# Performance work log

Measured on AMD Instinct MI355X. Metric: run time of the kernel, lower is better.

The kernel has to match this reference:

```python
import jax, jax.numpy as jnp
import numpy as np

B, NK, TK, H = 16, 2048, 4096, 256


def setup_inputs() -> dict:
    key = jax.random.key(0)
    ks = jax.random.split(key, 9)
    s = 0.02  # init scale for weights
    return {
        "s_t_hat": jax.random.normal(ks[0], (B, 2 * H), dtype=jnp.float32),
        "encoder_outputs_node": jax.random.normal(ks[1], (B, NK, H), dtype=jnp.float32),
        "node_to_token": jax.random.uniform(ks[2], (B, NK, TK), dtype=jnp.float32),
        "enc_padding_mask_node": jnp.ones((B, NK), dtype=jnp.float32),
        "graph": jax.random.uniform(ks[3], (B, NK, NK), dtype=jnp.float32),
        "flow": jax.random.uniform(ks[4], (B, NK), dtype=jnp.float32),
        "W_c_w": jax.random.normal(ks[5], (1, H), dtype=jnp.float32) * s,
        "enc_proj_w": jax.random.normal(ks[6], (H, H), dtype=jnp.float32) * s,
        "dec_proj_w": jax.random.normal(ks[7], (2 * H, H), dtype=jnp.float32) * s,
        "dec_proj_b": jnp.zeros((H,), dtype=jnp.float32),
        "v_node_w": jax.random.normal(ks[8], (H, 1), dtype=jnp.float32) * s,
    }


def reference(s_t_hat, encoder_outputs_node, node_to_token, enc_padding_mask_node,
              graph, flow, W_c_w, enc_proj_w, dec_proj_w, dec_proj_b, v_node_w):
    # additive attention scoring over graph nodes
    enc_feat = jnp.einsum('bkh,hd->bkd', encoder_outputs_node, enc_proj_w)   # (b,nk,h)
    dec_fea = s_t_hat @ dec_proj_w + dec_proj_b                              # (b,h)
    _flow_feature = flow[..., None] @ W_c_w  # computed in original but unused (dead code)
    e = jnp.tanh(enc_feat + dec_fea[:, None, :])                             # (b,nk,h)
    scores = jnp.squeeze(e @ v_node_w, -1)                                   # (b,nk)
    # masked softmax with renormalization
    attn_ = jax.nn.softmax(scores, axis=1) * enc_padding_mask_node
    attn = attn_ / jnp.sum(attn_, axis=1, keepdims=True)                     # (b,nk)
    # project node attention to token space, renormalize
    tok_ = jnp.einsum('bk,bkt->bt', attn, node_to_token)                     # (b,tk)
    tok = tok_ / jnp.sum(tok_, axis=1, keepdims=True)
    # context vector
    c_t = jnp.einsum('bk,bkh->bh', attn, encoder_outputs_node)               # (b,h)
    # multi-hop graph diffusion
    one_hop = jnp.einsum('bk,bkm->bm', attn, graph)                          # (b,nk)
    two_hop = jnp.einsum('bk,bkm->bm', one_hop, graph)                       # (b,nk)
    flow_out = attn * 0.33333 + one_hop * 0.33333 + two_hop * 0.33333        # (b,nk)
    return (c_t, attn, tok, flow_out)
```

## Files before the change

### kernel.cpp

```cpp
#include <hip/hip_runtime.h>
#include <cstddef>

#define BB 16
#define NK 2048
#define TK 4096
#define HH 256
#define H2 512

__global__ void k_dec_fea(const float* __restrict__ s_t_hat,
                          const float* __restrict__ Wd,
                          const float* __restrict__ bd,
                          float* __restrict__ dec_fea) {
    int b = blockIdx.x, d = threadIdx.x;
    __shared__ float s[H2];
    s[d]       = s_t_hat[b * H2 + d];
    s[d + HH]  = s_t_hat[b * H2 + HH + d];
    __syncthreads();
    float acc = bd[d];
    #pragma unroll 8
    for (int j = 0; j < H2; ++j) acc = fmaf(s[j], Wd[j * HH + d], acc);
    dec_fea[b * HH + d] = acc;
}

__global__ void k_scores(const float* __restrict__ enc,
                         const float* __restrict__ Wenc,
                         const float* __restrict__ dec_fea,
                         const float* __restrict__ v,
                         float* __restrict__ scores) {
    int b   = blockIdx.y;
    int k0  = blockIdx.x * 16;
    int tid = threadIdx.x;
    int lane = tid & 63;
    int wv   = tid >> 6;

    __shared__ float4 encSV[16 * 64];
    const float4* baseV = (const float4*)(enc + ((size_t)b * NK + k0) * HH);
    #pragma unroll
    for (int r = 0; r < 4; ++r) encSV[r * 256 + tid] = baseV[r * 256 + tid];
    __syncthreads();

    const float4* Wv = (const float4*)Wenc;
    float4 acc[4];
    #pragma unroll
    for (int i = 0; i < 4; ++i) acc[i] = make_float4(0.f, 0.f, 0.f, 0.f);

    for (int h4 = 0; h4 < 64; ++h4) {
        float4 w0 = Wv[(h4 * 4 + 0) * 64 + lane];
        float4 w1 = Wv[(h4 * 4 + 1) * 64 + lane];
        float4 w2 = Wv[(h4 * 4 + 2) * 64 + lane];
        float4 w3 = Wv[(h4 * 4 + 3) * 64 + lane];
        #pragma unroll
        for (int i = 0; i < 4; ++i) {
            float4 e = encSV[(wv * 4 + i) * 64 + h4];
            acc[i].x = fmaf(e.x, w0.x, acc[i].x); acc[i].y = fmaf(e.x, w0.y, acc[i].y);
            acc[i].z = fmaf(e.x, w0.z, acc[i].z); acc[i].w = fmaf(e.x, w0.w, acc[i].w);
            acc[i].x = fmaf(e.y, w1.x, acc[i].x); acc[i].y = fmaf(e.y, w1.y, acc[i].y);
            acc[i].z = fmaf(e.y, w1.z, acc[i].z); acc[i].w = fmaf(e.y, w1.w, acc[i].w);
            acc[i].x = fmaf(e.z, w2.x, acc[i].x); acc[i].y = fmaf(e.z, w2.y, acc[i].y);
            acc[i].z = fmaf(e.z, w2.z, acc[i].z); acc[i].w = fmaf(e.z, w2.w, acc[i].w);
            acc[i].x = fmaf(e.w, w3.x, acc[i].x); acc[i].y = fmaf(e.w, w3.y, acc[i].y);
            acc[i].z = fmaf(e.w, w3.z, acc[i].z); acc[i].w = fmaf(e.w, w3.w, acc[i].w);
        }
    }

    float4 df = ((const float4*)(dec_fea + b * HH))[lane];
    float4 vv = ((const float4*)v)[lane];
    #pragma unroll
    for (int i = 0; i < 4; ++i) {
        float p = tanhf(acc[i].x + df.x) * vv.x
                + tanhf(acc[i].y + df.y) * vv.y
                + tanhf(acc[i].z + df.z) * vv.z
                + tanhf(acc[i].w + df.w) * vv.w;
        #pragma unroll
        for (int off = 32; off > 0; off >>= 1) p += __shfl_down(p, off, 64);
        if (lane == 0) scores[b * NK + k0 + wv * 4 + i] = p;
    }
}

__global__ void k_softmax(const float* __restrict__ scores,
                          const float* __restrict__ mask,
                          float* __restrict__ attn) {
    int b = blockIdx.x, tid = threadIdx.x;
    int lane = tid & 63, wv = tid >> 6;
    __shared__ float redmax[4], redsum[4];
    float vals[8];
    float m = -1e30f;
    #pragma unroll
    for (int r = 0; r < 8; ++r) {
        vals[r] = scores[b * NK + r * 256 + tid];
        m = fmaxf(m, vals[r]);
    }
    #pragma unroll
    for (int off = 1; off < 64; off <<= 1) m = fmaxf(m, __shfl_xor(m, off, 64));
    if (lane == 0) redmax[wv] = m;
    __syncthreads();
    m = fmaxf(fmaxf(redmax[0], redmax[1]), fmaxf(redmax[2], redmax[3]));
    float s = 0.f;
    #pragma unroll
    for (int r = 0; r < 8; ++r) {
        float e = __expf(vals[r] - m) * mask[b * NK + r * 256 + tid];
        vals[r] = e;
        s += e;
    }
    #pragma unroll
    for (int off = 1; off < 64; off <<= 1) s += __shfl_xor(s, off, 64);
    if (lane == 0) redsum[wv] = s;
    __syncthreads();
    s = redsum[0] + redsum[1] + redsum[2] + redsum[3];
    float inv = 1.f / s;
    #pragma unroll
    for (int r = 0; r < 8; ++r) attn[b * NK + r * 256 + tid] = vals[r] * inv;
}

__global__ void k_ct(const float* __restrict__ attn,
                     const float* __restrict__ enc,
                     float* __restrict__ out) {
    int b = blockIdx.y;
    int k0 = blockIdx.x * 64;
    int h = threadIdx.x;
    const float* e  = enc + ((size_t)b * NK + k0) * HH;
    const float* wb = attn + b * NK + k0;
    float acc = 0.f;
    #pragma unroll 8
    for (int k = 0; k < 64; ++k) acc = fmaf(wb[k], e[(size_t)k * HH + h], acc);
    atomicAdd(&out[b * HH + h], acc);
}

template <int NCOLS, int KCH>
__global__ void k_vecmat(const float* __restrict__ w,
                         const float* __restrict__ M,
                         float* __restrict__ out) {
    int b  = blockIdx.z;
    int k0 = blockIdx.y * (NK / KCH);
    int t  = blockIdx.x * 1024 + threadIdx.x * 4;
    const float4* Mv = (const float4*)(M + (size_t)b * NK * NCOLS);
    const float* wb  = w + b * NK;
    float4 acc = make_float4(0.f, 0.f, 0.f, 0.f);
    int kend = k0 + NK / KCH;
    #pragma unroll 4
    for (int k = k0; k < kend; ++k) {
        float a = wb[k];
        float4 vv = Mv[(size_t)k * (NCOLS / 4) + (t >> 2)];
        acc.x = fmaf(a, vv.x, acc.x);
        acc.y = fmaf(a, vv.y, acc.y);
        acc.z = fmaf(a, vv.z, acc.z);
        acc.w = fmaf(a, vv.w, acc.w);
    }
    float* o = out + b * NCOLS + t;
    atomicAdd(o + 0, acc.x);
    atomicAdd(o + 1, acc.y);
    atomicAdd(o + 2, acc.z);
    atomicAdd(o + 3, acc.w);
}

__global__ void k_flowout(const float* __restrict__ attn,
                          const float* __restrict__ oh,
                          const float* __restrict__ th,
                          float* __restrict__ out) {
    int i = blockIdx.x * 256 + threadIdx.x;
    out[i] = (attn[i] + oh[i] + th[i]) * 0.33333f;
}

__global__ void k_toknorm(const float* __restrict__ tok_raw,
                          float* __restrict__ out) {
    int b = blockIdx.x, tid = threadIdx.x;
    int lane = tid & 63, wv = tid >> 6;
    __shared__ float redsum[4];
    float vals[16];
    float s = 0.f;
    #pragma unroll
    for (int r = 0; r < 16; ++r) {
        vals[r] = tok_raw[b * TK + r * 256 + tid];
        s += vals[r];
    }
    #pragma unroll
    for (int off = 1; off < 64; off <<= 1) s += __shfl_xor(s, off, 64);
    if (lane == 0) redsum[wv] = s;
    __syncthreads();
    s = redsum[0] + redsum[1] + redsum[2] + redsum[3];
    float inv = 1.f / s;
    #pragma unroll
    for (int r = 0; r < 16; ++r) out[b * TK + r * 256 + tid] = vals[r] * inv;
}

extern "C" void kernel_launch(void* const* d_in, const int* in_sizes, int n_in,
                              void* d_out, int out_size, void* d_ws, size_t ws_size,
                              hipStream_t stream) {
    const float* s_t_hat = (const float*)d_in[0];
    const float* enc     = (const float*)d_in[1];
    const float* n2t     = (const float*)d_in[2];
    const float* mask    = (const float*)d_in[3];
    const float* graph   = (const float*)d_in[4];
    const float* Wenc    = (const float*)d_in[7];
    const float* Wdec    = (const float*)d_in[8];
    const float* bdec    = (const float*)d_in[9];
    const float* vnode   = (const float*)d_in[10];

    float* out = (float*)d_out;
    float* ws  = (float*)d_ws;

    float* dec_fea = ws;
    float* scores  = ws + 4096;
    float* tok_raw = ws + 36864;
    float* one_hop = ws + 102400;
    float* two_hop = ws + 135168;

    float* c_t   = out;
    float* attn  = out + 4096;
    float* tok   = out + 36864;
    float* flowo = out + 102400;

    hipMemsetAsync(c_t, 0, 4096 * sizeof(float), stream);
    hipMemsetAsync(tok_raw, 0, (65536 + 32768 + 32768) * sizeof(float), stream);

    k_dec_fea<<<BB, 256, 0, stream>>>(s_t_hat, Wdec, bdec, dec_fea);
    k_scores<<<dim3(NK / 16, BB), 256, 0, stream>>>(enc, Wenc, dec_fea, vnode, scores);
    k_softmax<<<BB, 256, 0, stream>>>(scores, mask, attn);
    k_ct<<<dim3(32, BB), 256, 0, stream>>>(attn, enc, c_t);
    k_vecmat<NK, 16><<<dim3(2, 16, BB), 256, 0, stream>>>(attn, graph, one_hop);
    k_vecmat<NK, 16><<<dim3(2, 16, BB), 256, 0, stream>>>(one_hop, graph, two_hop);
    k_vecmat<TK, 8><<<dim3(4, 8, BB), 256, 0, stream>>>(attn, n2t, tok_raw);
    k_flowout<<<(BB * NK) / 256, 256, 0, stream>>>(attn, one_hop, two_hop, flowo);
    k_toknorm<<<BB, 256, 0, stream>>>(tok_raw, tok);
}
```

Before: 1.018 ms.

## Split dec_fea across K, enlarge score tiles, stage vecmat weights in LDS

k_dec_fea is split over eight K-chunks per batch and accumulated with atomics into a zeroed buffer, which gives the tiny projection more blocks. k_scores now processes 32 nodes per block with eight accumulators per wave, so each Wenc load is reused across twice as many rows at the cost of higher register pressure. k_vecmat stages its weight slice in shared memory, and the graph and node_to_token launches use twice as many K-chunks, adding parallelism for these bandwidth-bound passes but doubling the atomic traffic. The tok vecmat launch is also moved after flowout.

Result: no change. 1.006 ms (-1.2%).

```diff
diff --git a/kernel.cpp b/kernel.cpp
--- a/kernel.cpp
+++ b/kernel.cpp
@@ -11,38 +11,39 @@
                           const float* __restrict__ Wd,
                           const float* __restrict__ bd,
                           float* __restrict__ dec_fea) {
-    int b = blockIdx.x, d = threadIdx.x;
-    __shared__ float s[H2];
-    s[d]       = s_t_hat[b * H2 + d];
-    s[d + HH]  = s_t_hat[b * H2 + HH + d];
-    __syncthreads();
-    float acc = bd[d];
-    #pragma unroll 8
-    for (int j = 0; j < H2; ++j) acc = fmaf(s[j], Wd[j * HH + d], acc);
-    dec_fea[b * HH + d] = acc;
-}
-
-__global__ void k_scores(const float* __restrict__ enc,
+    int b = blockIdx.x, ks = blockIdx.y;
+    int d = threadIdx.x;
+    __shared__ float s[64];
+    if (d < 64) s[d] = s_t_hat[b * H2 + ks * 64 + d];
+    __syncthreads();
+    float acc = (ks == 0) ? bd[d] : 0.f;
+    #pragma unroll
+    for (int j = 0; j < 64; ++j)
+        acc = fmaf(s[j], Wd[(ks * 64 + j) * HH + d], acc);
+    atomicAdd(&dec_fea[b * HH + d], acc);
+}
+
+__global__ __launch_bounds__(256) void k_scores(const float* __restrict__ enc,
                          const float* __restrict__ Wenc,
                          const float* __restrict__ dec_fea,
                          const float* __restrict__ v,
                          float* __restrict__ scores) {
     int b   = blockIdx.y;
-    int k0  = blockIdx.x * 16;
+    int k0  = blockIdx.x * 32;
     int tid = threadIdx.x;
     int lane = tid & 63;
     int wv   = tid >> 6;
 
-    __shared__ float4 encSV[16 * 64];
+    __shared__ float4 encSV[32 * 64];
     const float4* baseV = (const float4*)(enc + ((size_t)b * NK + k0) * HH);
     #pragma unroll
-    for (int r = 0; r < 4; ++r) encSV[r * 256 + tid] = baseV[r * 256 + tid];
+    for (int r = 0; r < 8; ++r) encSV[r * 256 + tid] = baseV[r * 256 + tid];
     __syncthreads();
 
     const float4* Wv = (const float4*)Wenc;
-    float4 acc[4];
-    #pragma unroll
-    for (int i = 0; i < 4; ++i) acc[i] = make_float4(0.f, 0.f, 0.f, 0.f);
+    float4 acc[8];
+    #pragma unroll
+    for (int i = 0; i < 8; ++i) acc[i] = make_float4(0.f, 0.f, 0.f, 0.f);
 
     for (int h4 = 0; h4 < 64; ++h4) {
         float4 w0 = Wv[(h4 * 4 + 0) * 64 + lane];
@@ -50,8 +51,8 @@
         float4 w2 = Wv[(h4 * 4 + 2) * 64 + lane];
         float4 w3 = Wv[(h4 * 4 + 3) * 64 + lane];
         #pragma unroll
-        for (int i = 0; i < 4; ++i) {
-            float4 e = encSV[(wv * 4 + i) * 64 + h4];
+        for (int i = 0; i < 8; ++i) {
+            float4 e = encSV[(wv * 8 + i) * 64 + h4];
             acc[i].x = fmaf(e.x, w0.x, acc[i].x); acc[i].y = fmaf(e.x, w0.y, acc[i].y);
             acc[i].z = fmaf(e.x, w0.z, acc[i].z); acc[i].w = fmaf(e.x, w0.w, acc[i].w);
             acc[i].x = fmaf(e.y, w1.x, acc[i].x); acc[i].y = fmaf(e.y, w1.y, acc[i].y);
@@ -66,14 +67,14 @@
     float4 df = ((const float4*)(dec_fea + b * HH))[lane];
     float4 vv = ((const float4*)v)[lane];
     #pragma unroll
-    for (int i = 0; i < 4; ++i) {
+    for (int i = 0; i < 8; ++i) {
         float p = tanhf(acc[i].x + df.x) * vv.x
                 + tanhf(acc[i].y + df.y) * vv.y
                 + tanhf(acc[i].z + df.z) * vv.z
                 + tanhf(acc[i].w + df.w) * vv.w;
         #pragma unroll
         for (int off = 32; off > 0; off >>= 1) p += __shfl_down(p, off, 64);
-        if (lane == 0) scores[b * NK + k0 + wv * 4 + i] = p;
+        if (lane == 0) scores[b * NK + k0 + wv * 8 + i] = p;
     }
 }
 
@@ -127,20 +128,23 @@
 }
 
 template <int NCOLS, int KCH>
-__global__ void k_vecmat(const float* __restrict__ w,
+__global__ __launch_bounds__(256) void k_vecmat(const float* __restrict__ w,
                          const float* __restrict__ M,
                          float* __restrict__ out) {
+    constexpr int KR = NK / KCH;
     int b  = blockIdx.z;
-    int k0 = blockIdx.y * (NK / KCH);
+    int k0 = blockIdx.y * KR;
     int t  = blockIdx.x * 1024 + threadIdx.x * 4;
-    const float4* Mv = (const float4*)(M + (size_t)b * NK * NCOLS);
-    const float* wb  = w + b * NK;
+    __shared__ float sw[KR];
+    for (int i = threadIdx.x; i < KR; i += 256) sw[i] = w[b * NK + k0 + i];
+    __syncthreads();
+    const float4* Mv = (const float4*)(M + (size_t)b * NK * NCOLS
+                                         + (size_t)k0 * NCOLS) + (t >> 2);
     float4 acc = make_float4(0.f, 0.f, 0.f, 0.f);
-    int kend = k0 + NK / KCH;
-    #pragma unroll 4
-    for (int k = k0; k < kend; ++k) {
-        float a = wb[k];
-        float4 vv = Mv[(size_t)k * (NCOLS / 4) + (t >> 2)];
+    #pragma unroll 8
+    for (int k = 0; k < KR; ++k) {
+        float a = sw[k];
+        float4 vv = Mv[(size_t)k * (NCOLS / 4)];
         acc.x = fmaf(a, vv.x, acc.x);
         acc.y = fmaf(a, vv.y, acc.y);
         acc.z = fmaf(a, vv.z, acc.z);
@@ -210,16 +214,17 @@
     float* tok   = out + 36864;
     float* flowo = out + 102400;
 
+    hipMemsetAsync(dec_fea, 0, 4096 * sizeof(float), stream);
     hipMemsetAsync(c_t, 0, 4096 * sizeof(float), stream);
     hipMemsetAsync(tok_raw, 0, (65536 + 32768 + 32768) * sizeof(float), stream);
 
-    k_dec_fea<<<BB, 256, 0, stream>>>(s_t_hat, Wdec, bdec, dec_fea);
-    k_scores<<<dim3(NK / 16, BB), 256, 0, stream>>>(enc, Wenc, dec_fea, vnode, scores);
+    k_dec_fea<<<dim3(BB, 8), 256, 0, stream>>>(s_t_hat, Wdec, bdec, dec_fea);
+    k_scores<<<dim3(NK / 32, BB), 256, 0, stream>>>(enc, Wenc, dec_fea, vnode, scores);
     k_softmax<<<BB, 256, 0, stream>>>(scores, mask, attn);
     k_ct<<<dim3(32, BB), 256, 0, stream>>>(attn, enc, c_t);
-    k_vecmat<NK, 16><<<dim3(2, 16, BB), 256, 0, stream>>>(attn, graph, one_hop);
-    k_vecmat<NK, 16><<<dim3(2, 16, BB), 256, 0, stream>>>(one_hop, graph, two_hop);
-    k_vecmat<TK, 8><<<dim3(4, 8, BB), 256, 0, stream>>>(attn, n2t, tok_raw);
+    k_vecmat<NK, 32><<<dim3(2, 32, BB), 256, 0, stream>>>(attn, graph, one_hop);
+    k_vecmat<NK, 32><<<dim3(2, 32, BB), 256, 0, stream>>>(one_hop, graph, two_hop);
     k_flowout<<<(BB * NK) / 256, 256, 0, stream>>>(attn, one_hop, two_hop, flowo);
+    k_vecmat<TK, 16><<<dim3(4, 16, BB), 256, 0, stream>>>(attn, n2t, tok_raw);
     k_toknorm<<<BB, 256, 0, stream>>>(tok_raw, tok);
 }
```
